# Optimization experiments

Hardware: AMD Instinct MI355X
Metric: run time of the kernel (lower is better)

The kernel has to match this reference:

```python
import jax, jax.numpy as jnp
import numpy as np

N_HITS = 100_000
D_EMB = 12
N_OBJ = 1024          # object ids 1..N_OBJ, id 0 = noise (noise_threshold=0)
Q_MIN = 0.1
SB = 0.1
MAX_N_REP = 100_000
EPS = 1e-9


def setup_inputs() -> dict:
    key = jax.random.key(0)
    k1, k2, k3 = jax.random.split(key, 3)
    # beta in (0, 0.95) so arctanh stays finite (torch code asserts no NaN in q)
    beta = jax.random.uniform(k1, (N_HITS,), jnp.float32) * 0.95
    # scale embeddings so a realistic fraction of pairs has dist < 1 (repulsion active)
    x = jax.random.normal(k2, (N_HITS, D_EMB), jnp.float32) * 0.3
    object_id = jax.random.randint(k3, (N_HITS,), 0, N_OBJ + 1).astype(jnp.int64)
    return {"beta": beta, "x": x, "object_id": object_id}


def reference(beta, x, object_id):
    n = beta.shape[0]
    oids = jnp.arange(1, N_OBJ + 1)                      # [K] (all non-noise ids present w.h.p.)
    att = object_id[:, None] == oids[None, :]            # [N,K] attractive mask

    q = jnp.arctanh(beta) ** 2 + Q_MIN                   # [N] charge
    alphas = jnp.argmax(q[:, None] * att, axis=0)        # [K] condensation point per object
    x_a = x[alphas]                                      # [K,d]
    q_a = q[alphas]                                      # [K]

    # pairwise squared distances [N,K] (cdist)
    d2 = (jnp.sum(x * x, axis=1)[:, None]
          - 2.0 * (x @ x_a.T)
          + jnp.sum(x_a * x_a, axis=1)[None, :])
    d2 = jnp.maximum(d2, 0.0)
    dist = jnp.sqrt(jnp.maximum(d2, 1e-12))              # safe sqrt (grad-safe)

    qw = q[:, None] * q_a[None, :]                       # [N,K] q_j * q_alpha_k

    # attractive: mean over hits of q_j * sum_k M_jk * q_k * d^2  (use d2, not dist**2)
    v_att = jnp.sum(jnp.where(att, qw * d2, 0.0)) / n

    # repulsive hinge, capped via random subsampling with 1/freq upweighting
    rep = (~att) & (dist < 1.0)
    n_rep_k = jnp.sum(rep)
    freq = jnp.minimum(
        jnp.float32(MAX_N_REP) / jnp.maximum(n_rep_k, 1).astype(jnp.float32), 1.0)
    samp = jax.random.uniform(jax.random.key(42), dist.shape) < freq
    rep = rep & samp
    v_rep = jnp.sum(jnp.where(rep, qw * (1.0 - dist), 0.0)) / freq / n

    # coward: push condensation-point betas toward 1
    l_coward = jnp.mean(1.0 - beta[alphas])

    # noise: mean beta over noise hits (object_id <= noise_threshold=0)
    noise_mask = object_id <= 0
    l_noise = jnp.sum(jnp.where(noise_mask, beta, 0.0)) / (
        jnp.maximum(jnp.sum(noise_mask), 1).astype(beta.dtype) + EPS)

    loss = v_att + v_rep + l_coward + l_noise * SB
    return jnp.stack([v_att, v_rep, l_coward, l_noise, loss])
```

## Files before the change

kernel.cpp:

```cpp
#include <hip/hip_runtime.h>
#include <stdint.h>

#define NHITS 100000
#define NOBJ  1024
#define HALF  50000
#define QUART 25000
#define HALF_PAIRS 51200000u


#define MASK_OFF 873792ull
#define WS_NEED (MASK_OFF + 16ull * NHITS * 8ull)

__device__ inline uint32_t rotl32(uint32_t x, int n) {
    return (x << n) | (x >> (32 - n));
}

__device__ inline void threefry2x32(uint32_t k0, uint32_t k1,
                                    uint32_t x0, uint32_t x1,
                                    uint32_t& o0, uint32_t& o1) {
    uint32_t ks2 = k0 ^ k1 ^ 0x1BD11BDAu;
    x0 += k0; x1 += k1;
#define TF_ROUND(r) { x0 += x1; x1 = rotl32(x1, r); x1 ^= x0; }
    TF_ROUND(13) TF_ROUND(15) TF_ROUND(26) TF_ROUND(6)
    x0 += k1;  x1 += ks2 + 1u;
    TF_ROUND(17) TF_ROUND(29) TF_ROUND(16) TF_ROUND(24)
    x0 += ks2; x1 += k0 + 2u;
    TF_ROUND(13) TF_ROUND(15) TF_ROUND(26) TF_ROUND(6)
    x0 += k0;  x1 += k1 + 3u;
    TF_ROUND(17) TF_ROUND(29) TF_ROUND(16) TF_ROUND(24)
    x0 += k1;  x1 += ks2 + 4u;
    TF_ROUND(13) TF_ROUND(15) TF_ROUND(26) TF_ROUND(6)
    x0 += ks2; x1 += k0 + 5u;
#undef TF_ROUND
    o0 = x0; o1 = x1;
}

__device__ inline float tf_uniform(uint32_t bits) {
    return __uint_as_float((bits >> 9) | 0x3f800000u) - 1.0f;
}

__device__ inline double waveReduceD(double v) {
    for (int off = 32; off > 0; off >>= 1) v += __shfl_down(v, off, 64);
    return v;
}
__device__ inline unsigned int waveReduceU(unsigned int v) {
    for (int off = 32; off > 0; off >>= 1) v += __shfl_down(v, off, 64);
    return v;
}

#define DOT12(XA, XB, XC, A, B, C) \
    fmaf((XC).w, (C).w, fmaf((XC).z, (C).z, fmaf((XC).y, (C).y, fmaf((XC).x, (C).x, \
    fmaf((XB).w, (B).w, fmaf((XB).z, (B).z, fmaf((XB).y, (B).y, fmaf((XB).x, (B).x, \
    fmaf((XA).w, (A).w, fmaf((XA).z, (A).z, fmaf((XA).y, (A).y, (XA).x * (A).x)))))))))))

#define SS12(XA, XB, XC) DOT12(XA, XB, XC, XA, XB, XC)


__global__ void k_init(unsigned long long* packed, unsigned long long* hdr) {
    int t = blockIdx.x * blockDim.x + threadIdx.x;
    if (t < NOBJ) packed[t] = 0xFFFFFFFFull;
    if (t < 8)    hdr[t] = 0ull;
}

__global__ void k_hits(const float* __restrict__ beta,
                       const float* __restrict__ x,
                       const int* __restrict__ oid,
                       unsigned long long* __restrict__ packed,
                       float* __restrict__ q_arr,
                       float* __restrict__ xx_arr,
                       double* __restrict__ noise_sum,
                       unsigned long long* __restrict__ noise_cnt) {
    int j = blockIdx.x * blockDim.x + threadIdx.x;
    float nb = 0.0f;
    unsigned int nc = 0;
    if (j < NHITS) {
        float b = beta[j];
        int o = oid[j];
        float a = atanhf(b);
        float q = a * a + 0.1f;
        q_arr[j] = q;
        const float4* x4 = (const float4*)x;
        float4 A = x4[j * 3 + 0], B = x4[j * 3 + 1], C = x4[j * 3 + 2];
        xx_arr[j] = SS12(A, B, C);
        if (o > 0) {
            unsigned long long p =
                ((unsigned long long)__float_as_uint(q) << 32) |
                (unsigned long long)(0xFFFFFFFFu - (unsigned)j);
            atomicMax(&packed[o - 1], p);
        } else {
            nb = b; nc = 1;
        }
    }
    double rb = waveReduceD((double)nb);
    unsigned int rc = waveReduceU(nc);
    if ((threadIdx.x & 63) == 0) {
        if (rb != 0.0) atomicAdd(noise_sum, rb);
        if (rc)        atomicAdd(noise_cnt, (unsigned long long)rc);
    }
}

__global__ void k_alphas(const unsigned long long* __restrict__ packed,
                         const float* __restrict__ x,
                         const float* __restrict__ beta,
                         const float* __restrict__ q_arr,
                         const float* __restrict__ xx_arr,
                         float* __restrict__ arec,
                         double* __restrict__ coward_sum) {
    int k = blockIdx.x * blockDim.x + threadIdx.x;
    double c = 0.0;
    if (k < NOBJ) {
        unsigned idx = 0xFFFFFFFFu - (unsigned)(packed[k] & 0xFFFFFFFFull);
        const float4* x4 = (const float4*)x;
        float4 A = x4[idx * 3 + 0];
        float4 B = x4[idx * 3 + 1];
        float4 C = x4[idx * 3 + 2];
        float4 D;
        D.x = q_arr[idx]; D.y = xx_arr[idx]; D.z = 0.f; D.w = 0.f;
        float4* ar = (float4*)arec;
        ar[k * 4 + 0] = A;
        ar[k * 4 + 1] = B;
        ar[k * 4 + 2] = C;
        ar[k * 4 + 3] = D;
        c = 1.0 - (double)beta[idx];
    }
    double rc = waveReduceD(c);
    if ((threadIdx.x & 63) == 0) atomicAdd(coward_sum, rc);
}

__global__ void k_att(const float* __restrict__ x,
                      const int* __restrict__ oid,
                      const float* __restrict__ q_arr,
                      const float* __restrict__ xx_arr,
                      const float* __restrict__ arec,
                      double* __restrict__ v_att_sum) {
    int j = blockIdx.x * blockDim.x + threadIdx.x;
    double va = 0.0;
    if (j < NHITS) {
        int o = oid[j];
        if (o > 0) {
            int k = o - 1;
            const float4* x4 = (const float4*)x;
            float4 XA = x4[j * 3 + 0], XB = x4[j * 3 + 1], XC = x4[j * 3 + 2];
            const float4* ar = (const float4*)arec;
            float4 A = ar[k * 4 + 0], B = ar[k * 4 + 1], C = ar[k * 4 + 2], D = ar[k * 4 + 3];
            float dot = DOT12(XA, XB, XC, A, B, C);
            float d2r = fmaf(-2.0f, dot, xx_arr[j]) + D.y;
            va = (double)((q_arr[j] * D.x) * fmaxf(d2r, 0.0f));
        }
    }
    double rv = waveReduceD(va);
    if ((threadIdx.x & 63) == 0) {
        if (rv != 0.0) atomicAdd(v_att_sum, rv);
    }
}

__global__ __launch_bounds__(256)
void k_scan(const float* __restrict__ x,
            const float* __restrict__ xx_arr,
            const int* __restrict__ oid,
            const float* __restrict__ arec,
            unsigned long long* __restrict__ mb64,
            unsigned int* __restrict__ nrep,
            int do_write) {
    __shared__ float4 spack[64 * 4];
    __shared__ unsigned int su[4];
    const int tid = threadIdx.x;
    const int kb = blockIdx.y * 64;
    const float4* ar4 = (const float4*)arec;
    spack[tid] = ar4[kb * 4 + tid];
    __syncthreads();

    const int t = blockIdx.x * 256 + tid;
    const bool valid = t < QUART;
    const int j0 = valid ? t : 0;
    const int j1 = j0 + QUART;
    const int j2 = j0 + 2 * QUART;
    const int j3 = j0 + 3 * QUART;
    const float4* x4 = (const float4*)x;

    float4 X0a = x4[j0 * 3 + 0], X0b = x4[j0 * 3 + 1], X0c = x4[j0 * 3 + 2];
    float4 X1a = x4[j1 * 3 + 0], X1b = x4[j1 * 3 + 1], X1c = x4[j1 * 3 + 2];
    float4 X2a = x4[j2 * 3 + 0], X2b = x4[j2 * 3 + 1], X2c = x4[j2 * 3 + 2];
    float4 X3a = x4[j3 * 3 + 0], X3b = x4[j3 * 3 + 1], X3c = x4[j3 * 3 + 2];

    const float inval = valid ? 0.0f : 3e9f;
    const float xx0 = xx_arr[j0] + inval;
    const float xx1 = xx_arr[j1] + inval;
    const float xx2 = xx_arr[j2] + inval;
    const float xx3 = xx_arr[j3] + inval;
    const int o0 = valid ? oid[j0] : 0;
    const int o1 = valid ? oid[j1] : 0;
    const int o2 = valid ? oid[j2] : 0;
    const int o3 = valid ? oid[j3] : 0;

    uint32_t mA0 = 0, mA1 = 0, mB0 = 0, mB1 = 0;
    uint32_t mC0 = 0, mC1 = 0, mD0 = 0, mD1 = 0;

#define SCANH(BASE, MA, MB, MC, MD)                                         \
    {                                                                       \
        uint32_t bit = 1u;                                                  \
        for (int kk = 0; kk < 32; ++kk, bit += bit) {                       \
            int kl = (BASE) + kk;                                           \
            float4 A = spack[kl * 4 + 0];                                   \
            float4 B = spack[kl * 4 + 1];                                   \
            float4 C = spack[kl * 4 + 2];                                   \
            float a2 = spack[kl * 4 + 3].y;                                 \
            float d0 = DOT12(X0a, X0b, X0c, A, B, C);                       \
            float d1 = DOT12(X1a, X1b, X1c, A, B, C);                       \
            float d2 = DOT12(X2a, X2b, X2c, A, B, C);                       \
            float d3 = DOT12(X3a, X3b, X3c, A, B, C);                       \
            float t0 = fmaf(-2.0f, d0, xx0) + a2;                           \
            float t1 = fmaf(-2.0f, d1, xx1) + a2;                           \
            float t2 = fmaf(-2.0f, d2, xx2) + a2;                           \
            float t3 = fmaf(-2.0f, d3, xx3) + a2;                           \
            MA |= (t0 < 1.0f) ? bit : 0u;                                   \
            MB |= (t1 < 1.0f) ? bit : 0u;                                   \
            MC |= (t2 < 1.0f) ? bit : 0u;                                   \
            MD |= (t3 < 1.0f) ? bit : 0u;                                   \
        }                                                                   \
    }
    SCANH(0,  mA0, mB0, mC0, mD0)
    SCANH(32, mA1, mB1, mC1, mD1)
#undef SCANH

#define CLR_ATT(O, LO, HI)                                                  \
    if ((O) > 0) {                                                          \
        int rel = (O) - 1 - kb;                                             \
        if (rel >= 0 && rel < 64) {                                         \
            uint32_t b = ~(1u << (rel & 31));                               \
            if (rel < 32) LO &= b; else HI &= b;                            \
        }                                                                   \
    }
    CLR_ATT(o0, mA0, mA1)
    CLR_ATT(o1, mB0, mB1)
    CLR_ATT(o2, mC0, mC1)
    CLR_ATT(o3, mD0, mD1)
#undef CLR_ATT

    const unsigned long long M0 = (unsigned long long)mA0 | ((unsigned long long)mA1 << 32);
    const unsigned long long M1 = (unsigned long long)mB0 | ((unsigned long long)mB1 << 32);
    const unsigned long long M2 = (unsigned long long)mC0 | ((unsigned long long)mC1 << 32);
    const unsigned long long M3 = (unsigned long long)mD0 | ((unsigned long long)mD1 << 32);

    if (do_write && valid) {
        const size_t W = (size_t)blockIdx.y;
        mb64[W * NHITS + j0] = M0;
        mb64[W * NHITS + j1] = M1;
        mb64[W * NHITS + j2] = M2;
        mb64[W * NHITS + j3] = M3;
    }

    unsigned int cnt = (unsigned)(__popcll(M0) + __popcll(M1) +
                                  __popcll(M2) + __popcll(M3));
    unsigned int rc = waveReduceU(cnt);
    if ((tid & 63) == 0) su[tid >> 6] = rc;
    __syncthreads();
    if (tid == 0) {
        unsigned int s = su[0] + su[1] + su[2] + su[3];
        if (s) atomicAdd(nrep, s);
    }
}

__global__ void k_freq(const unsigned int* __restrict__ nrep,
                       float* __restrict__ freq) {
    unsigned int n = *nrep;
    if (n < 1u) n = 1u;
    float f = 100000.0f / (float)n;
    *freq = fminf(f, 1.0f);
}

__global__ __launch_bounds__(256)
void k_rep(const float* __restrict__ x,
           const float* __restrict__ q_arr,
           const float* __restrict__ xx_arr,
           const float* __restrict__ arec,
           const unsigned long long* __restrict__ mb64,
           const float* __restrict__ freq_ptr,
           double* __restrict__ acc_out) {
    __shared__ unsigned short qq[4][4096];
    __shared__ double sd[4];
    const int tid = threadIdx.x;
    const int lane = tid & 63;
    const int w = tid >> 6;
    const int W = blockIdx.y;
    const int jblk = blockIdx.x * 1024;
    const float freq = *freq_ptr;
    const float4* x4 = (const float4*)x;
    const float4* ar = (const float4*)arec;
    double acc = 0.0;

    for (int r = 0; r < 4; ++r) {
        const int jround = jblk + r * 256 + (w << 6);
        const int j = jround + lane;
        unsigned long long m = (j < NHITS) ? mb64[(size_t)W * NHITS + j] : 0ull;
        unsigned int cnt = (unsigned)__popcll(m);

        unsigned int p = cnt;
#pragma unroll
        for (int off = 1; off < 64; off <<= 1) {
            unsigned int v = __shfl_up(p, off, 64);
            if (lane >= off) p += v;
        }
        const unsigned int excl = p - cnt;
        const unsigned int T = __shfl(p, 63, 64);

        {
            unsigned long long mm = m;
            unsigned int pos = excl;
            unsigned short base = (unsigned short)(lane << 6);
            while (mm) {
                int b = (int)__builtin_ctzll(mm);
                mm &= mm - 1ull;
                qq[w][pos++] = (unsigned short)(base | (unsigned short)b);
            }
        }
        __syncthreads();

        for (unsigned int i = lane; i < T; i += 64) {
            int desc = (int)qq[w][i];
            int jj = jround + (desc >> 6);
            int k = (W << 6) + (desc & 63);
            uint32_t f = (uint32_t)jj * NOBJ + (uint32_t)k;
            bool lo = jj < HALF;
            uint32_t xa = lo ? f : (f - HALF_PAIRS);
            uint32_t r0, r1;
            threefry2x32(0u, 42u, xa, xa + HALF_PAIRS, r0, r1);
            float u = tf_uniform(lo ? r0 : r1);
            if (u < freq) {
                float4 XA = x4[jj * 3 + 0], XB = x4[jj * 3 + 1], XC = x4[jj * 3 + 2];
                float4 A = ar[k * 4 + 0], B = ar[k * 4 + 1];
                float4 C = ar[k * 4 + 2], D = ar[k * 4 + 3];
                float dot = DOT12(XA, XB, XC, A, B, C);
                float d2 = fmaf(-2.0f, dot, xx_arr[jj]) + D.y;
                float dist = sqrtf(fmaxf(fmaxf(d2, 0.0f), 1e-12f));
                acc += (double)((q_arr[jj] * D.x) * (1.0f - dist));
            }
        }
        __syncthreads();
    }

    double rv = waveReduceD(acc);
    if (lane == 0) sd[w] = rv;
    __syncthreads();
    if (tid == 0) {
        double s = sd[0] + sd[1] + sd[2] + sd[3];
        if (s != 0.0) atomicAdd(acc_out, s);
    }
}

__global__ __launch_bounds__(256)
void k_rep_fb(const float* __restrict__ x,
              const float* __restrict__ q_arr,
              const float* __restrict__ xx_arr,
              const int* __restrict__ oid,
              const float* __restrict__ arec,
              const float* __restrict__ freq_ptr,
              double* __restrict__ acc_out) {
    __shared__ double sacc[4];
    const int tid = threadIdx.x;
    int t = blockIdx.x * 256 + tid;
    bool valid = t < HALF;
    int j0 = valid ? t : 0;
    int j1 = j0 + HALF;
    const float4* x4 = (const float4*)x;
    float4 X0a = x4[j0 * 3 + 0], X0b = x4[j0 * 3 + 1], X0c = x4[j0 * 3 + 2];
    float4 X1a = x4[j1 * 3 + 0], X1b = x4[j1 * 3 + 1], X1c = x4[j1 * 3 + 2];
    float xx0 = valid ? xx_arr[j0] : 3e9f;
    float xx1 = valid ? xx_arr[j1] : 3e9f;
    int o0 = oid[j0], o1 = oid[j1];
    const float4* ar = (const float4*)arec;
    const int kb = blockIdx.y * 128;
    const float freq = *freq_ptr;

    double acc = 0.0;
#define FB_G(G, J, XA, XB, XC, XX, OO, S1)                                      \
    {                                                                           \
        uint32_t m = 0, bit = 1u;                                               \
        int kbase = kb + (G) * 32;                                              \
        for (int kk = 0; kk < 32; ++kk, bit += bit) {                           \
            int k = kbase + kk;                                                 \
            float4 A = ar[k * 4 + 0];                                           \
            float4 B = ar[k * 4 + 1];                                           \
            float4 C = ar[k * 4 + 2];                                           \
            float a2 = ar[k * 4 + 3].y;                                         \
            float d0 = DOT12(XA, XB, XC, A, B, C);                              \
            float t0 = fmaf(-2.0f, d0, XX) + a2;                                \
            m |= (t0 < 1.0f && (OO) != k + 1) ? bit : 0u;                       \
        }                                                                       \
        while (m) {                                                             \
            int kk = __ffs(m) - 1; m &= m - 1;                                  \
            int k = kbase + kk;                                                 \
            uint32_t f = (uint32_t)(J) * NOBJ + (uint32_t)k;                    \
            uint32_t xa_ = (S1) ? (f - HALF_PAIRS) : f;                         \
            uint32_t b0_, b1_;                                                  \
            threefry2x32(0u, 42u, xa_, xa_ + HALF_PAIRS, b0_, b1_);             \
            float u = tf_uniform((S1) ? b1_ : b0_);                             \
            if (u < freq) {                                                     \
                float4 A = ar[k * 4 + 0], B = ar[k * 4 + 1], C = ar[k * 4 + 2], D = ar[k * 4 + 3]; \
                float dot = DOT12(XA, XB, XC, A, B, C);                         \
                float d2 = fmaf(-2.0f, dot, XX) + D.y;                          \
                float dist = sqrtf(fmaxf(fmaxf(d2, 0.0f), 1e-12f));             \
                acc += (double)((q_arr[J] * D.x) * (1.0f - dist));              \
            }                                                                   \
        }                                                                       \
    }
    FB_G(0, j0, X0a, X0b, X0c, xx0, o0, false)
    FB_G(1, j0, X0a, X0b, X0c, xx0, o0, false)
    FB_G(2, j0, X0a, X0b, X0c, xx0, o0, false)
    FB_G(3, j0, X0a, X0b, X0c, xx0, o0, false)
    FB_G(0, j1, X1a, X1b, X1c, xx1, o1, true)
    FB_G(1, j1, X1a, X1b, X1c, xx1, o1, true)
    FB_G(2, j1, X1a, X1b, X1c, xx1, o1, true)
    FB_G(3, j1, X1a, X1b, X1c, xx1, o1, true)
#undef FB_G

    double rv = waveReduceD(acc);
    if ((tid & 63) == 0) sacc[tid >> 6] = rv;
    __syncthreads();
    if (tid == 0) {
        double s = sacc[0] + sacc[1] + sacc[2] + sacc[3];
        if (s != 0.0) atomicAdd(acc_out, s);
    }
}

__global__ void k_final(const double* __restrict__ accs,
                        const unsigned long long* __restrict__ noise_cnt,
                        const float* __restrict__ freq,
                        float* __restrict__ out) {
    double v_att = accs[0] / (double)NHITS;
    double v_rep = accs[1] / (double)(*freq) / (double)NHITS;
    double l_cow = accs[2] / (double)NOBJ;
    unsigned long long nc = *noise_cnt;
    if (nc < 1ull) nc = 1ull;
    double l_noise = accs[3] / ((double)nc + 1e-9);
    double loss = v_att + v_rep + l_cow + 0.1 * l_noise;
    out[0] = (float)v_att;
    out[1] = (float)v_rep;
    out[2] = (float)l_cow;
    out[3] = (float)l_noise;
    out[4] = (float)loss;
}


extern "C" void kernel_launch(void* const* d_in, const int* in_sizes, int n_in,
                              void* d_out, int out_size, void* d_ws, size_t ws_size,
                              hipStream_t stream) {
    const float* beta = (const float*)d_in[0];
    const float* x    = (const float*)d_in[1];
    const int*   oid  = (const int*)d_in[2];
    float* out = (float*)d_out;

    char* ws = (char*)d_ws;
    double* v_att_sum = (double*)(ws + 0);
    double* v_rep_sum = (double*)(ws + 8);
    double* coward_sum = (double*)(ws + 16);
    double* noise_sum = (double*)(ws + 24);
    unsigned long long* noise_cnt = (unsigned long long*)(ws + 32);
    unsigned int* nrep = (unsigned int*)(ws + 40);
    float* freq = (float*)(ws + 48);
    unsigned long long* packed = (unsigned long long*)(ws + 64);
    float* arec = (float*)(ws + 8256);
    float* q_arr = (float*)(ws + 73792);
    float* xx_arr = (float*)(ws + 473792);
    unsigned long long* mb64 = (unsigned long long*)(ws + MASK_OFF);

    const int wsok = (ws_size >= WS_NEED) ? 1 : 0;

    k_init<<<4, 256, 0, stream>>>(packed, (unsigned long long*)ws);
    k_hits<<<(NHITS + 255) / 256, 256, 0, stream>>>(beta, x, oid, packed,
                                                    q_arr, xx_arr,
                                                    noise_sum, noise_cnt);
    k_alphas<<<4, 256, 0, stream>>>(packed, x, beta, q_arr, xx_arr,
                                    arec, coward_sum);

    dim3 gs((QUART + 255) / 256, 16);
    k_scan<<<gs, 256, 0, stream>>>(x, xx_arr, oid, arec, mb64, nrep, wsok);

    k_att<<<(NHITS + 255) / 256, 256, 0, stream>>>(x, oid, q_arr, xx_arr,
                                                   arec, v_att_sum);
    k_freq<<<1, 1, 0, stream>>>(nrep, freq);

    if (wsok) {
        dim3 gr((NHITS + 1023) / 1024, 16);
        k_rep<<<gr, 256, 0, stream>>>(x, q_arr, xx_arr, arec, mb64,
                                      freq, v_rep_sum);
    } else {
        dim3 gfb((HALF + 255) / 256, 8);
        k_rep_fb<<<gfb, 256, 0, stream>>>(x, q_arr, xx_arr, oid, arec,
                                          freq, v_rep_sum);
    }

    k_final<<<1, 1, 0, stream>>>((double*)ws, noise_cnt, freq, out);
}
```

Baseline: 143.8 us.

## Fuse attractive term into scan, pack FMAs, drop freq kernel

Removes the separate k_att kernel by computing each hit's attractive term inside k_scan, where its own condensation point already sits in shared memory. Also drops the single-thread k_freq launch; the frequency is recomputed from nrep inside each consumer. The scan's dot products now run on 2-wide float vectors so the compiler can emit packed FP32 FMAs, pairing hits j0/j1 and j2/j3. The aim is fewer launches and higher FMA throughput, at the cost of extra vector registers and a second reduction in k_scan.

```diff
diff --git a/kernel.cpp b/kernel.cpp
--- a/kernel.cpp
+++ b/kernel.cpp
@@ -6,6 +6,8 @@
 #define HALF  50000
 #define QUART 25000
 #define HALF_PAIRS 51200000u
+
+typedef float v2f __attribute__((ext_vector_type(2)));
 
 
 #define MASK_OFF 873792ull
@@ -37,6 +39,11 @@
 
 __device__ inline float tf_uniform(uint32_t bits) {
     return __uint_as_float((bits >> 9) | 0x3f800000u) - 1.0f;
+}
+
+__device__ inline float freq_from_n(unsigned int n) {
+    if (n < 1u) n = 1u;
+    return fminf(100000.0f / (float)n, 1.0f);
 }
 
 __device__ inline double waveReduceD(double v) {
@@ -127,43 +134,19 @@
     if ((threadIdx.x & 63) == 0) atomicAdd(coward_sum, rc);
 }
 
-__global__ void k_att(const float* __restrict__ x,
-                      const int* __restrict__ oid,
-                      const float* __restrict__ q_arr,
-                      const float* __restrict__ xx_arr,
-                      const float* __restrict__ arec,
-                      double* __restrict__ v_att_sum) {
-    int j = blockIdx.x * blockDim.x + threadIdx.x;
-    double va = 0.0;
-    if (j < NHITS) {
-        int o = oid[j];
-        if (o > 0) {
-            int k = o - 1;
-            const float4* x4 = (const float4*)x;
-            float4 XA = x4[j * 3 + 0], XB = x4[j * 3 + 1], XC = x4[j * 3 + 2];
-            const float4* ar = (const float4*)arec;
-            float4 A = ar[k * 4 + 0], B = ar[k * 4 + 1], C = ar[k * 4 + 2], D = ar[k * 4 + 3];
-            float dot = DOT12(XA, XB, XC, A, B, C);
-            float d2r = fmaf(-2.0f, dot, xx_arr[j]) + D.y;
-            va = (double)((q_arr[j] * D.x) * fmaxf(d2r, 0.0f));
-        }
-    }
-    double rv = waveReduceD(va);
-    if ((threadIdx.x & 63) == 0) {
-        if (rv != 0.0) atomicAdd(v_att_sum, rv);
-    }
-}
-
 __global__ __launch_bounds__(256)
 void k_scan(const float* __restrict__ x,
+            const float* __restrict__ q_arr,
             const float* __restrict__ xx_arr,
             const int* __restrict__ oid,
             const float* __restrict__ arec,
             unsigned long long* __restrict__ mb64,
             unsigned int* __restrict__ nrep,
+            double* __restrict__ v_att_sum,
             int do_write) {
     __shared__ float4 spack[64 * 4];
     __shared__ unsigned int su[4];
+    __shared__ double sd[4];
     const int tid = threadIdx.x;
     const int kb = blockIdx.y * 64;
     const float4* ar4 = (const float4*)arec;
@@ -183,11 +166,22 @@
     float4 X2a = x4[j2 * 3 + 0], X2b = x4[j2 * 3 + 1], X2c = x4[j2 * 3 + 2];
     float4 X3a = x4[j3 * 3 + 0], X3b = x4[j3 * 3 + 1], X3c = x4[j3 * 3 + 2];
 
+    v2f hp0 = (v2f){X0a.x, X1a.x}, hp1 = (v2f){X0a.y, X1a.y};
+    v2f hp2 = (v2f){X0a.z, X1a.z}, hp3 = (v2f){X0a.w, X1a.w};
+    v2f hp4 = (v2f){X0b.x, X1b.x}, hp5 = (v2f){X0b.y, X1b.y};
+    v2f hp6 = (v2f){X0b.z, X1b.z}, hp7 = (v2f){X0b.w, X1b.w};
+    v2f hp8 = (v2f){X0c.x, X1c.x}, hp9 = (v2f){X0c.y, X1c.y};
+    v2f hp10 = (v2f){X0c.z, X1c.z}, hp11 = (v2f){X0c.w, X1c.w};
+    v2f hq0 = (v2f){X2a.x, X3a.x}, hq1 = (v2f){X2a.y, X3a.y};
+    v2f hq2 = (v2f){X2a.z, X3a.z}, hq3 = (v2f){X2a.w, X3a.w};
+    v2f hq4 = (v2f){X2b.x, X3b.x}, hq5 = (v2f){X2b.y, X3b.y};
+    v2f hq6 = (v2f){X2b.z, X3b.z}, hq7 = (v2f){X2b.w, X3b.w};
+    v2f hq8 = (v2f){X2c.x, X3c.x}, hq9 = (v2f){X2c.y, X3c.y};
+    v2f hq10 = (v2f){X2c.z, X3c.z}, hq11 = (v2f){X2c.w, X3c.w};
+
     const float inval = valid ? 0.0f : 3e9f;
-    const float xx0 = xx_arr[j0] + inval;
-    const float xx1 = xx_arr[j1] + inval;
-    const float xx2 = xx_arr[j2] + inval;
-    const float xx3 = xx_arr[j3] + inval;
+    v2f xxP = (v2f){xx_arr[j0] + inval, xx_arr[j1] + inval};
+    v2f xxQ = (v2f){xx_arr[j2] + inval, xx_arr[j3] + inval};
     const int o0 = valid ? oid[j0] : 0;
     const int o1 = valid ? oid[j1] : 0;
     const int o2 = valid ? oid[j2] : 0;
@@ -205,37 +199,76 @@
             float4 B = spack[kl * 4 + 1];                                   \
             float4 C = spack[kl * 4 + 2];                                   \
             float a2 = spack[kl * 4 + 3].y;                                 \
-            float d0 = DOT12(X0a, X0b, X0c, A, B, C);                       \
-            float d1 = DOT12(X1a, X1b, X1c, A, B, C);                       \
-            float d2 = DOT12(X2a, X2b, X2c, A, B, C);                       \
-            float d3 = DOT12(X3a, X3b, X3c, A, B, C);                       \
-            float t0 = fmaf(-2.0f, d0, xx0) + a2;                           \
-            float t1 = fmaf(-2.0f, d1, xx1) + a2;                           \
-            float t2 = fmaf(-2.0f, d2, xx2) + a2;                           \
-            float t3 = fmaf(-2.0f, d3, xx3) + a2;                           \
-            MA |= (t0 < 1.0f) ? bit : 0u;                                   \
-            MB |= (t1 < 1.0f) ? bit : 0u;                                   \
-            MC |= (t2 < 1.0f) ? bit : 0u;                                   \
-            MD |= (t3 < 1.0f) ? bit : 0u;                                   \
+            v2f dP = hp0 * (v2f){A.x, A.x};                                 \
+            v2f dQ = hq0 * (v2f){A.x, A.x};                                 \
+            dP = __builtin_elementwise_fma(hp1,  (v2f){A.y, A.y}, dP);      \
+            dQ = __builtin_elementwise_fma(hq1,  (v2f){A.y, A.y}, dQ);      \
+            dP = __builtin_elementwise_fma(hp2,  (v2f){A.z, A.z}, dP);      \
+            dQ = __builtin_elementwise_fma(hq2,  (v2f){A.z, A.z}, dQ);      \
+            dP = __builtin_elementwise_fma(hp3,  (v2f){A.w, A.w}, dP);      \
+            dQ = __builtin_elementwise_fma(hq3,  (v2f){A.w, A.w}, dQ);      \
+            dP = __builtin_elementwise_fma(hp4,  (v2f){B.x, B.x}, dP);      \
+            dQ = __builtin_elementwise_fma(hq4,  (v2f){B.x, B.x}, dQ);      \
+            dP = __builtin_elementwise_fma(hp5,  (v2f){B.y, B.y}, dP);      \
+            dQ = __builtin_elementwise_fma(hq5,  (v2f){B.y, B.y}, dQ);      \
+            dP = __builtin_elementwise_fma(hp6,  (v2f){B.z, B.z}, dP);      \
+            dQ = __builtin_elementwise_fma(hq6,  (v2f){B.z, B.z}, dQ);      \
+            dP = __builtin_elementwise_fma(hp7,  (v2f){B.w, B.w}, dP);      \
+            dQ = __builtin_elementwise_fma(hq7,  (v2f){B.w, B.w}, dQ);      \
+            dP = __builtin_elementwise_fma(hp8,  (v2f){C.x, C.x}, dP);      \
+            dQ = __builtin_elementwise_fma(hq8,  (v2f){C.x, C.x}, dQ);      \
+            dP = __builtin_elementwise_fma(hp9,  (v2f){C.y, C.y}, dP);      \
+            dQ = __builtin_elementwise_fma(hq9,  (v2f){C.y, C.y}, dQ);      \
+            dP = __builtin_elementwise_fma(hp10, (v2f){C.z, C.z}, dP);      \
+            dQ = __builtin_elementwise_fma(hq10, (v2f){C.z, C.z}, dQ);      \
+            dP = __builtin_elementwise_fma(hp11, (v2f){C.w, C.w}, dP);      \
+            dQ = __builtin_elementwise_fma(hq11, (v2f){C.w, C.w}, dQ);      \
+            v2f eP = __builtin_elementwise_fma((v2f){-2.f, -2.f}, dP, xxP); \
+            v2f eQ = __builtin_elementwise_fma((v2f){-2.f, -2.f}, dQ, xxQ); \
+            eP = eP + (v2f){a2, a2};                                        \
+            eQ = eQ + (v2f){a2, a2};                                        \
+            MA |= (eP[0] < 1.0f) ? bit : 0u;                                \
+            MB |= (eP[1] < 1.0f) ? bit : 0u;                                \
+            MC |= (eQ[0] < 1.0f) ? bit : 0u;                                \
+            MD |= (eQ[1] < 1.0f) ? bit : 0u;                                \
         }                                                                   \
     }
     SCANH(0,  mA0, mB0, mC0, mD0)
     SCANH(32, mA1, mB1, mC1, mD1)
 #undef SCANH
 
-#define CLR_ATT(O, LO, HI)                                                  \
+    double vatt = 0.0;
+#define ATT_SLOT(O, J, H, S, XXV, LO, HI)                                   \
     if ((O) > 0) {                                                          \
         int rel = (O) - 1 - kb;                                             \
         if (rel >= 0 && rel < 64) {                                         \
-            uint32_t b = ~(1u << (rel & 31));                               \
-            if (rel < 32) LO &= b; else HI &= b;                            \
+            uint32_t bb = ~(1u << (rel & 31));                              \
+            if (rel < 32) LO &= bb; else HI &= bb;                          \
+            float4 A = spack[rel * 4 + 0];                                  \
+            float4 B = spack[rel * 4 + 1];                                  \
+            float4 C = spack[rel * 4 + 2];                                  \
+            float4 D = spack[rel * 4 + 3];                                  \
+            float dot = H##0[S] * A.x;                                      \
+            dot = fmaf(H##1[S],  A.y, dot);                                 \
+            dot = fmaf(H##2[S],  A.z, dot);                                 \
+            dot = fmaf(H##3[S],  A.w, dot);                                 \
+            dot = fmaf(H##4[S],  B.x, dot);                                 \
+            dot = fmaf(H##5[S],  B.y, dot);                                 \
+            dot = fmaf(H##6[S],  B.z, dot);                                 \
+            dot = fmaf(H##7[S],  B.w, dot);                                 \
+            dot = fmaf(H##8[S],  C.x, dot);                                 \
+            dot = fmaf(H##9[S],  C.y, dot);                                 \
+            dot = fmaf(H##10[S], C.z, dot);                                 \
+            dot = fmaf(H##11[S], C.w, dot);                                 \
+            float d2r = fmaf(-2.0f, dot, XXV) + D.y;                        \
+            vatt += (double)((q_arr[J] * D.x) * fmaxf(d2r, 0.0f));          \
         }                                                                   \
     }
-    CLR_ATT(o0, mA0, mA1)
-    CLR_ATT(o1, mB0, mB1)
-    CLR_ATT(o2, mC0, mC1)
-    CLR_ATT(o3, mD0, mD1)
-#undef CLR_ATT
+    ATT_SLOT(o0, j0, hp, 0, xxP[0], mA0, mA1)
+    ATT_SLOT(o1, j1, hp, 1, xxP[1], mB0, mB1)
+    ATT_SLOT(o2, j2, hq, 0, xxQ[0], mC0, mC1)
+    ATT_SLOT(o3, j3, hq, 1, xxQ[1], mD0, mD1)
+#undef ATT_SLOT
 
     const unsigned long long M0 = (unsigned long long)mA0 | ((unsigned long long)mA1 << 32);
     const unsigned long long M1 = (unsigned long long)mB0 | ((unsigned long long)mB1 << 32);
@@ -253,20 +286,15 @@
     unsigned int cnt = (unsigned)(__popcll(M0) + __popcll(M1) +
                                   __popcll(M2) + __popcll(M3));
     unsigned int rc = waveReduceU(cnt);
-    if ((tid & 63) == 0) su[tid >> 6] = rc;
+    double rv = waveReduceD(vatt);
+    if ((tid & 63) == 0) { su[tid >> 6] = rc; sd[tid >> 6] = rv; }
     __syncthreads();
     if (tid == 0) {
         unsigned int s = su[0] + su[1] + su[2] + su[3];
         if (s) atomicAdd(nrep, s);
-    }
-}
-
-__global__ void k_freq(const unsigned int* __restrict__ nrep,
-                       float* __restrict__ freq) {
-    unsigned int n = *nrep;
-    if (n < 1u) n = 1u;
-    float f = 100000.0f / (float)n;
-    *freq = fminf(f, 1.0f);
+        double v = sd[0] + sd[1] + sd[2] + sd[3];
+        if (v != 0.0) atomicAdd(v_att_sum, v);
+    }
 }
 
 __global__ __launch_bounds__(256)
@@ -275,7 +303,7 @@
            const float* __restrict__ xx_arr,
            const float* __restrict__ arec,
            const unsigned long long* __restrict__ mb64,
-           const float* __restrict__ freq_ptr,
+           const unsigned int* __restrict__ nrep,
            double* __restrict__ acc_out) {
     __shared__ unsigned short qq[4][4096];
     __shared__ double sd[4];
@@ -284,7 +312,7 @@
     const int w = tid >> 6;
     const int W = blockIdx.y;
     const int jblk = blockIdx.x * 1024;
-    const float freq = *freq_ptr;
+    const float freq = freq_from_n(*nrep);
     const float4* x4 = (const float4*)x;
     const float4* ar = (const float4*)arec;
     double acc = 0.0;
@@ -354,7 +382,7 @@
               const float* __restrict__ xx_arr,
               const int* __restrict__ oid,
               const float* __restrict__ arec,
-              const float* __restrict__ freq_ptr,
+              const unsigned int* __restrict__ nrep,
               double* __restrict__ acc_out) {
     __shared__ double sacc[4];
     const int tid = threadIdx.x;
@@ -370,7 +398,7 @@
     int o0 = oid[j0], o1 = oid[j1];
     const float4* ar = (const float4*)arec;
     const int kb = blockIdx.y * 128;
-    const float freq = *freq_ptr;
+    const float freq = freq_from_n(*nrep);
 
     double acc = 0.0;
 #define FB_G(G, J, XA, XB, XC, XX, OO, S1)                                      \
@@ -425,10 +453,11 @@
 
 __global__ void k_final(const double* __restrict__ accs,
                         const unsigned long long* __restrict__ noise_cnt,
-                        const float* __restrict__ freq,
+                        const unsigned int* __restrict__ nrep,
                         float* __restrict__ out) {
+    float freq = freq_from_n(*nrep);
     double v_att = accs[0] / (double)NHITS;
-    double v_rep = accs[1] / (double)(*freq) / (double)NHITS;
+    double v_rep = accs[1] / (double)freq / (double)NHITS;
     double l_cow = accs[2] / (double)NOBJ;
     unsigned long long nc = *noise_cnt;
     if (nc < 1ull) nc = 1ull;
@@ -457,7 +486,6 @@
     double* noise_sum = (double*)(ws + 24);
     unsigned long long* noise_cnt = (unsigned long long*)(ws + 32);
     unsigned int* nrep = (unsigned int*)(ws + 40);
-    float* freq = (float*)(ws + 48);
     unsigned long long* packed = (unsigned long long*)(ws + 64);
     float* arec = (float*)(ws + 8256);
     float* q_arr = (float*)(ws + 73792);
@@ -474,21 +502,18 @@
                                     arec, coward_sum);
 
     dim3 gs((QUART + 255) / 256, 16);
-    k_scan<<<gs, 256, 0, stream>>>(x, xx_arr, oid, arec, mb64, nrep, wsok);
-
-    k_att<<<(NHITS + 255) / 256, 256, 0, stream>>>(x, oid, q_arr, xx_arr,
-                                                   arec, v_att_sum);
-    k_freq<<<1, 1, 0, stream>>>(nrep, freq);
+    k_scan<<<gs, 256, 0, stream>>>(x, q_arr, xx_arr, oid, arec,
+                                   mb64, nrep, v_att_sum, wsok);
 
     if (wsok) {
         dim3 gr((NHITS + 1023) / 1024, 16);
         k_rep<<<gr, 256, 0, stream>>>(x, q_arr, xx_arr, arec, mb64,
-                                      freq, v_rep_sum);
+                                      nrep, v_rep_sum);
     } else {
         dim3 gfb((HALF + 255) / 256, 8);
         k_rep_fb<<<gfb, 256, 0, stream>>>(x, q_arr, xx_arr, oid, arec,
-                                          freq, v_rep_sum);
-    }
-
-    k_final<<<1, 1, 0, stream>>>((double*)ws, noise_cnt, freq, out);
-}
+                                          nrep, v_rep_sum);
+    }
+
+    k_final<<<1, 1, 0, stream>>>((double*)ws, noise_cnt, nrep, out);
+}
```

Measured after the change: 131.5 us. -8.6%, faster.
